# Kernel optimization log

Measured on AMD Instinct MI355X. Metric: run time of the kernel, lower is better.

The kernel has to match this reference:

```python
import jax, jax.numpy as jnp
import numpy as np

D_MODEL = 1024
N_HEADS = 16
HEAD_DIM = D_MODEL // N_HEADS
D_FF = 4096
EPS = 1e-5
THETA = 10000.0
B, S = 2, 2048


def _rope_cache(seq_len, head_dim, theta=THETA):
    inv_freq = 1.0 / theta ** (jnp.arange(0, head_dim, 2, dtype=jnp.float32) / head_dim)
    t = jnp.arange(seq_len, dtype=jnp.float32)
    freqs = jnp.einsum('i,j->ij', t, inv_freq)          # [S, head_dim//2]
    emb = jnp.concatenate([freqs, freqs], axis=-1)       # [S, head_dim]
    return jnp.cos(emb), jnp.sin(emb)


def _rotate_half(x):
    x1, x2 = jnp.split(x, 2, axis=-1)
    return jnp.concatenate([-x2, x1], axis=-1)


def _ada_rmsnorm(x, time_emb, weight, w1, b1, w2, b2):
    # time_mlp: Linear -> SiLU -> Linear producing [B, 2*D]
    h = jax.nn.silu(time_emb @ w1 + b1)
    scale, shift = jnp.split(h @ w2 + b2, 2, axis=-1)    # each [B, D]
    norm = x * jax.lax.rsqrt(jnp.mean(x * x, axis=-1, keepdims=True) + EPS)
    return norm * weight * (1.0 + scale[:, None, :]) + shift[:, None, :]


def setup_inputs() -> dict:
    key = jax.random.key(0)
    ks = jax.random.split(key, 24)
    rn = lambda k, shp: (jax.random.normal(k, shp, dtype=jnp.float32) * 0.02)
    return {
        'x': jax.random.normal(ks[0], (B, S, D_MODEL), dtype=jnp.float32),
        'time_emb': jax.random.normal(ks[1], (B, D_MODEL), dtype=jnp.float32),
        # norm1
        'w_norm1': jnp.ones((D_MODEL,), jnp.float32),
        't1_w1': rn(ks[2], (D_MODEL, D_MODEL)), 't1_b1': jnp.zeros((D_MODEL,), jnp.float32),
        't1_w2': rn(ks[3], (D_MODEL, 2 * D_MODEL)), 't1_b2': jnp.zeros((2 * D_MODEL,), jnp.float32),
        # norm2
        'w_norm2': jnp.ones((D_MODEL,), jnp.float32),
        't2_w1': rn(ks[4], (D_MODEL, D_MODEL)), 't2_b1': jnp.zeros((D_MODEL,), jnp.float32),
        't2_w2': rn(ks[5], (D_MODEL, 2 * D_MODEL)), 't2_b2': jnp.zeros((2 * D_MODEL,), jnp.float32),
        # attention projections (stored [in, out])
        'wq': rn(ks[6], (D_MODEL, D_MODEL)), 'bq': jnp.zeros((D_MODEL,), jnp.float32),
        'wk': rn(ks[7], (D_MODEL, D_MODEL)), 'bk': jnp.zeros((D_MODEL,), jnp.float32),
        'wv': rn(ks[8], (D_MODEL, D_MODEL)), 'bv': jnp.zeros((D_MODEL,), jnp.float32),
        'wo': rn(ks[9], (D_MODEL, D_MODEL)), 'bo': jnp.zeros((D_MODEL,), jnp.float32),
        # GLU FFN (no bias)
        'w_gate': rn(ks[10], (D_MODEL, D_FF)),
        'w_up': rn(ks[11], (D_MODEL, D_FF)),
        'w_down': rn(ks[12], (D_FF, D_MODEL)),
    }


def reference(x, time_emb,
              w_norm1, t1_w1, t1_b1, t1_w2, t1_b2,
              w_norm2, t2_w1, t2_b1, t2_w2, t2_b2,
              wq, bq, wk, bk, wv, bv, wo, bo,
              w_gate, w_up, w_down):
    b, s, _ = x.shape
    cos, sin = _rope_cache(s, HEAD_DIM)                  # [S, head_dim]

    # --- attention sub-block ---
    nx = _ada_rmsnorm(x, time_emb, w_norm1, t1_w1, t1_b1, t1_w2, t1_b2)
    q = (nx @ wq + bq).reshape(b, s, N_HEADS, HEAD_DIM)
    k = (nx @ wk + bk).reshape(b, s, N_HEADS, HEAD_DIM)
    v = (nx @ wv + bv).reshape(b, s, N_HEADS, HEAD_DIM)
    c = cos[:, None, :]  # [S,1,head_dim] broadcasts over heads
    si = sin[:, None, :]
    q = q * c + _rotate_half(q) * si
    k = k * c + _rotate_half(k) * si
    scores = jnp.einsum('bshd,bthd->bhst', q, k) / jnp.sqrt(jnp.float32(HEAD_DIM))
    probs = jax.nn.softmax(scores, axis=-1)
    attn = jnp.einsum('bhst,bthd->bshd', probs, v).reshape(b, s, D_MODEL)
    x = x + attn @ wo + bo

    # --- GLU FFN sub-block ---
    nx = _ada_rmsnorm(x, time_emb, w_norm2, t2_w1, t2_b1, t2_w2, t2_b2)
    gate = jax.nn.gelu(nx @ w_gate, approximate=False)
    ff = (gate * (nx @ w_up)) @ w_down
    return x + ff
```

## Files before the change

### kernel.cpp

```cpp
#include <hip/hip_runtime.h>
#include <hip/hip_bf16.h>

typedef __bf16 bf16_t;
typedef __bf16 bf16x8 __attribute__((ext_vector_type(8)));
typedef float f32x4 __attribute__((ext_vector_type(4)));

typedef __attribute__((address_space(3))) void lds_void_t;
typedef const __attribute__((address_space(1))) void gbl_void_t;

static constexpr int S_LEN = 2048;
static constexpr int NBATCH = 2;
static constexpr int DM = 1024;
static constexpr int NH = 16;
static constexpr int HD = 64;
static constexpr int DFF = 4096;
static constexpr int MROWS = NBATCH * S_LEN;
static constexpr int QKVN = 3072;

__global__ __launch_bounds__(256) void rope_table_k(float* __restrict__ cs) {
  int idx = blockIdx.x * 256 + threadIdx.x;
  int i = idx & 31, s = idx >> 5;
  float inv = powf(10000.0f, -(float)i / 32.0f);
  float ang = (float)s * inv;
  float c = cosf(ang), sn = sinf(ang);
  cs[s * 64 + i] = c;  cs[s * 64 + i + 32] = c;
  cs[S_LEN * 64 + s * 64 + i] = sn;  cs[S_LEN * 64 + s * 64 + i + 32] = sn;
}

__global__ __launch_bounds__(256) void gemv_k(const float* __restrict__ vin,
    const float* __restrict__ W, const float* __restrict__ bias,
    float* __restrict__ out, int N, int dosilu) {
  int b = blockIdx.y;
  int tj = threadIdx.x & 31, ti = threadIdx.x >> 5;
  int j = blockIdx.x * 32 + tj;
  const float* v = vin + b * DM;
  float acc = 0.f;
  int i0 = ti * 128;
#pragma unroll 8
  for (int i = i0; i < i0 + 128; ++i) acc += v[i] * W[(size_t)i * N + j];
  __shared__ float red[8][32];
  red[ti][tj] = acc;
  __syncthreads();
  if (threadIdx.x < 32) {
    float a = 0.f;
#pragma unroll
    for (int t = 0; t < 8; ++t) a += red[t][threadIdx.x];
    a += bias[j - tj + threadIdx.x];
    if (dosilu) a = a / (1.0f + expf(-a));
    out[(size_t)b * N + blockIdx.x * 32 + threadIdx.x] = a;
  }
}

__global__ __launch_bounds__(256) void bcat_k(const float* __restrict__ bq,
    const float* __restrict__ bk, const float* __restrict__ bv, float* __restrict__ o) {
  int i = blockIdx.x * 256 + threadIdx.x;
  o[i] = i < 1024 ? bq[i] : (i < 2048 ? bk[i - 1024] : bv[i - 2048]);
}

template<typename T>
__global__ __launch_bounds__(256) void ada_rms_k(const T* __restrict__ x,
    const float* __restrict__ wnorm, const float* __restrict__ ss,
    bf16_t* __restrict__ out) {
  int row = blockIdx.x;
  int b = row >> 11;
  const T* xr = x + (size_t)row * DM;
  float xl[4]; float s = 0.f;
#pragma unroll
  for (int i = 0; i < 4; ++i) { xl[i] = (float)xr[threadIdx.x + i * 256]; s += xl[i] * xl[i]; }
#pragma unroll
  for (int d = 1; d < 64; d <<= 1) s += __shfl_xor(s, d);
  __shared__ float red[4];
  int w = threadIdx.x >> 6;
  if ((threadIdx.x & 63) == 0) red[w] = s;
  __syncthreads();
  s = red[0] + red[1] + red[2] + red[3];
  float r = rsqrtf(s * (1.0f / DM) + 1e-5f);
  bf16_t* orow = out + (size_t)row * DM;
#pragma unroll
  for (int i = 0; i < 4; ++i) {
    int j = threadIdx.x + i * 256;
    float sc = ss[b * 2048 + j], sh = ss[b * 2048 + 1024 + j];
    orow[j] = (bf16_t)(xl[i] * r * wnorm[j] * (1.0f + sc) + sh);
  }
}

__global__ __launch_bounds__(256) void conv_t_k(const float* __restrict__ in,
    bf16_t* __restrict__ out, int K, int N, int ilv) {
  __shared__ float t[32][33];
  int n0 = blockIdx.x * 32, k0 = blockIdx.y * 32;
  int tx = threadIdx.x & 31, ty = threadIdx.x >> 5;
#pragma unroll
  for (int i = 0; i < 32; i += 8)
    t[ty + i][tx] = in[(size_t)(k0 + ty + i) * N + n0 + tx];
  __syncthreads();
#pragma unroll
  for (int i = 0; i < 32; i += 8) {
    int n = n0 + ty + i;
    int row = (ilv == 0) ? n : ((n >> 4) * 32 + (n & 15) + (ilv == 2 ? 16 : 0));
    out[(size_t)row * K + k0 + tx] = (bf16_t)t[tx][ty + i];
  }
}

template<int EPI, int BK>
__global__ __launch_bounds__(256) void gemm_bt(
    const bf16_t* __restrict__ A, const bf16_t* __restrict__ BT,
    int M, int N, int K,
    const float* __restrict__ bias, const float* __restrict__ residf,
    const bf16_t* __restrict__ residb, bf16_t* outb, float* outf,
    const float* __restrict__ cstab, bf16_t* __restrict__ vt) {
  constexpr int DB = (BK == 64) ? 1 : 2;
  const int col0 = blockIdx.x * 128, row0 = blockIdx.y * 128;
  const int tid = threadIdx.x, l = tid & 63, w = tid >> 6;
  const int wr = (w >> 1) * 64, wc = (w & 1) * 64;
  const int lo = l & 15, hi = l >> 4;
  __shared__ __align__(16) bf16_t lA[DB][128][BK];
  __shared__ __align__(16) bf16_t lB[DB][128][BK];
  f32x4 zero = {0.f, 0.f, 0.f, 0.f};
  f32x4 acc[4][4];
#pragma unroll
  for (int m = 0; m < 4; ++m)
#pragma unroll
    for (int n = 0; n < 4; ++n) acc[m][n] = zero;

  auto stage = [&](int buf, int k0) {
    if constexpr (BK == 64) {
      const int lrow = l >> 3;
      const int swzb = ((l & 7) ^ lrow) * 16;
#pragma unroll
      for (int i = 0; i < 4; ++i) {
        int rbase = w * 32 + i * 8;
        const char* gA = (const char*)&A[(size_t)(row0 + rbase + lrow) * K + k0] + swzb;
        const char* gB = (const char*)&BT[(size_t)(col0 + rbase + lrow) * K + k0] + swzb;
        __builtin_amdgcn_global_load_lds((gbl_void_t*)gA, (lds_void_t*)&lA[buf][rbase][0], 16, 0, 0);
        __builtin_amdgcn_global_load_lds((gbl_void_t*)gB, (lds_void_t*)&lB[buf][rbase][0], 16, 0, 0);
      }
    } else {
      const int lrow = l >> 4;
#pragma unroll
      for (int i = 0; i < 8; ++i) {
        int rbase = w * 32 + i * 4;
        int key = (i * 4 + lrow) & 15;
        int swzb = ((l & 15) ^ key) * 16;
        const char* gA = (const char*)&A[(size_t)(row0 + rbase + lrow) * K + k0] + swzb;
        const char* gB = (const char*)&BT[(size_t)(col0 + rbase + lrow) * K + k0] + swzb;
        __builtin_amdgcn_global_load_lds((gbl_void_t*)gA, (lds_void_t*)&lA[buf][rbase][0], 16, 0, 0);
        __builtin_amdgcn_global_load_lds((gbl_void_t*)gB, (lds_void_t*)&lB[buf][rbase][0], 16, 0, 0);
      }
    }
  };

  const int cmask = (BK == 64) ? (lo & 7) : lo;
  const int NT = K / BK;

  auto compute = [&](int buf) {
#pragma unroll
    for (int kk = 0; kk < BK; kk += 32) {
      bf16x8 af[4], bfr[4];
#pragma unroll
      for (int m = 0; m < 4; ++m)
        af[m] = *(const bf16x8*)&lA[buf][wr + m * 16 + lo][(((kk >> 3) + hi) ^ cmask) * 8];
#pragma unroll
      for (int n = 0; n < 4; ++n)
        bfr[n] = *(const bf16x8*)&lB[buf][wc + n * 16 + lo][(((kk >> 3) + hi) ^ cmask) * 8];
#pragma unroll
      for (int m = 0; m < 4; ++m)
#pragma unroll
        for (int n = 0; n < 4; ++n)
          acc[m][n] = __builtin_amdgcn_mfma_f32_16x16x32_bf16(af[m], bfr[n], acc[m][n], 0, 0, 0);
    }
  };

  if constexpr (DB == 1) {
    for (int t = 0; t < NT; ++t) {
      __syncthreads();
      stage(0, t * BK);
      __syncthreads();
      compute(0);
    }
  } else {
    stage(0, 0);
    __syncthreads();
    int cur = 0;
    for (int t = 0; t < NT; ++t) {
      if (t + 1 < NT) stage(cur ^ 1, (t + 1) * BK);
      compute(cur);
      __syncthreads();
      cur ^= 1;
    }
  }

  if (EPI == 5) {
    if (col0 >= 2048) {
#pragma unroll
      for (int m = 0; m < 4; ++m) {
#pragma unroll
        for (int n = 0; n < 4; ++n) {
          int cl = col0 + wc + n * 16 + lo;
          int r0 = row0 + wr + m * 16 + hi * 4;
          int dfull = cl - 2048;
          int bh = (r0 >> 11) * 16 + (dfull >> 6);
          int d = dfull & 63;
          float bb = bias[cl];
          __align__(8) bf16_t tmp[4];
#pragma unroll
          for (int j = 0; j < 4; ++j) tmp[j] = (bf16_t)(acc[m][n][j] + bb);
          *(uint2*)&vt[((size_t)bh * 64 + d) * S_LEN + (r0 & 2047)] = *(uint2*)tmp;
        }
      }
    } else {
#pragma unroll
      for (int m = 0; m < 4; ++m) {
#pragma unroll
        for (int n = 0; n < 2; ++n) {
          int cl = col0 + wc + n * 16 + lo;
          int i = cl & 63;
          float b1 = bias[cl], b2 = bias[cl + 32];
          float scale = (cl < 1024) ? 0.125f : 1.0f;
#pragma unroll
          for (int j = 0; j < 4; ++j) {
            int r = row0 + wr + m * 16 + hi * 4 + j;
            int s = r & 2047;
            float c = cstab[s * 64 + i], sn = cstab[S_LEN * 64 + s * 64 + i];
            float x1 = acc[m][n][j] + b1, x2 = acc[m][n + 2][j] + b2;
            size_t idx = (size_t)r * N + cl;
            outb[idx]      = (bf16_t)((x1 * c - x2 * sn) * scale);
            outb[idx + 32] = (bf16_t)((x2 * c + x1 * sn) * scale);
          }
        }
      }
    }
    return;
  }

  if (EPI == 6) {
#pragma unroll
    for (int m = 0; m < 4; ++m) {
#pragma unroll
      for (int p = 0; p < 2; ++p) {
        int clg = col0 + wc + 2 * p * 16;
        int jcol = ((clg >> 5) << 4) + lo;
#pragma unroll
        for (int j = 0; j < 4; ++j) {
          int r = row0 + wr + m * 16 + hi * 4 + j;
          float g = acc[m][2 * p][j];
          float u = acc[m][2 * p + 1][j];
          g = 0.5f * g * (1.0f + erff(g * 0.70710678118f));
          outb[(size_t)r * DFF + jcol] = (bf16_t)(g * u);
        }
      }
    }
    return;
  }

#pragma unroll
  for (int m = 0; m < 4; ++m) {
#pragma unroll
    for (int n = 0; n < 4; ++n) {
#pragma unroll
      for (int j = 0; j < 4; ++j) {
        int r = row0 + wr + m * 16 + hi * 4 + j;
        int cl = col0 + wc + n * 16 + lo;
        size_t idx = (size_t)r * N + cl;
        float vv = acc[m][n][j];
        if (EPI == 1)      { vv += bias[cl] + residf[idx]; outb[idx] = (bf16_t)vv; }
        else               { vv += (float)residb[idx]; outf[idx] = vv; }
      }
    }
  }
}

__global__ __launch_bounds__(512, 4) void attn_k(const bf16_t* __restrict__ qk,
    const bf16_t* __restrict__ vt, bf16_t* __restrict__ o) {
  int g = blockIdx.x;
  int orig = (g & 7) * 64 + (g >> 3);
  int qblk = orig & 15;
  int bh = orig >> 4;
  int b = bh >> 4, h = bh & 15;
  const int q0 = qblk * 128;
  const int tid = threadIdx.x, l = tid & 63, w = tid >> 6;
  const int lo = l & 15, hi = l >> 4;

  __shared__ __align__(16) bf16_t lk[128][72];
  __shared__ __align__(16) bf16_t lvt[64][136];
  __shared__ __align__(16) bf16_t lp[8][16][136];

  bf16x8 qf[2];
#pragma unroll
  for (int ks = 0; ks < 2; ++ks)
    qf[ks] = *(const bf16x8*)&qk[((size_t)(b * S_LEN) + q0 + w * 16 + lo) * QKVN
                                 + h * HD + ks * 32 + hi * 8];

  f32x4 zero = {0.f, 0.f, 0.f, 0.f};
  f32x4 oa[4];
#pragma unroll
  for (int n = 0; n < 4; ++n) oa[n] = zero;
  float mrow[4], lrow[4];
#pragma unroll
  for (int j = 0; j < 4; ++j) { mrow[j] = -1e30f; lrow[j] = 0.f; }

  const size_t kbase = (size_t)(b * S_LEN) * QKVN + 1024 + h * HD;
  const size_t vbase = (size_t)bh * 64 * S_LEN;

  for (int t0 = 0; t0 < S_LEN; t0 += 128) {
    __syncthreads();
#pragma unroll
    for (int it = 0; it < 2; ++it) {
      int idx = it * 512 + tid;
      int r = idx >> 3, dc = (idx & 7) * 8;
      *(uint4*)&lk[r][dc] = *(const uint4*)&qk[kbase + (size_t)(t0 + r) * QKVN + dc];
      int d = idx >> 4, sc = (idx & 15) * 8;
      *(uint4*)&lvt[d][sc] = *(const uint4*)&vt[vbase + (size_t)d * S_LEN + t0 + sc];
    }
    __syncthreads();

    f32x4 s[8];
#pragma unroll
    for (int n = 0; n < 8; ++n) s[n] = zero;
    __builtin_amdgcn_s_setprio(1);
#pragma unroll
    for (int ks = 0; ks < 2; ++ks) {
#pragma unroll
      for (int n = 0; n < 8; ++n) {
        bf16x8 bk = *(const bf16x8*)&lk[n * 16 + lo][ks * 32 + hi * 8];
        s[n] = __builtin_amdgcn_mfma_f32_16x16x32_bf16(qf[ks], bk, s[n], 0, 0, 0);
      }
    }
    __builtin_amdgcn_s_setprio(0);

#pragma unroll
    for (int j = 0; j < 4; ++j) {
      float mx = fmaxf(fmaxf(fmaxf(s[0][j], s[1][j]), fmaxf(s[2][j], s[3][j])),
                       fmaxf(fmaxf(s[4][j], s[5][j]), fmaxf(s[6][j], s[7][j])));
      mx = fmaxf(mx, __shfl_xor(mx, 1));
      mx = fmaxf(mx, __shfl_xor(mx, 2));
      mx = fmaxf(mx, __shfl_xor(mx, 4));
      mx = fmaxf(mx, __shfl_xor(mx, 8));
      if (__any(mx > mrow[j] + 8.0f)) {
        float mn = fmaxf(mrow[j], mx);
        float corr = __expf(mrow[j] - mn);
        mrow[j] = mn;
        lrow[j] *= corr;
#pragma unroll
        for (int n = 0; n < 4; ++n) oa[n][j] *= corr;
      }
      float psum = 0.f;
#pragma unroll
      for (int n = 0; n < 8; ++n) {
        float p = __expf(s[n][j] - mrow[j]);
        psum += p;
        lp[w][hi * 4 + j][n * 16 + lo] = (bf16_t)p;
      }
      lrow[j] += psum;
    }

    __builtin_amdgcn_s_setprio(1);
#pragma unroll
    for (int kk = 0; kk < 128; kk += 32) {
      bf16x8 ap = *(const bf16x8*)&lp[w][lo][kk + hi * 8];
#pragma unroll
      for (int n = 0; n < 4; ++n) {
        bf16x8 bv = *(const bf16x8*)&lvt[n * 16 + lo][kk + hi * 8];
        oa[n] = __builtin_amdgcn_mfma_f32_16x16x32_bf16(ap, bv, oa[n], 0, 0, 0);
      }
    }
    __builtin_amdgcn_s_setprio(0);
  }

#pragma unroll
  for (int j = 0; j < 4; ++j) {
    float ls = lrow[j];
    ls += __shfl_xor(ls, 1); ls += __shfl_xor(ls, 2);
    ls += __shfl_xor(ls, 4); ls += __shfl_xor(ls, 8);
    float inv = 1.0f / ls;
    int row = q0 + w * 16 + hi * 4 + j;
#pragma unroll
    for (int n = 0; n < 4; ++n)
      o[((size_t)(b * S_LEN) + row) * DM + h * HD + n * 16 + lo] = (bf16_t)(oa[n][j] * inv);
  }
}

extern "C" void kernel_launch(void* const* d_in, const int* in_sizes, int n_in,
                              void* d_out, int out_size, void* d_ws, size_t ws_size,
                              hipStream_t stream) {
  const float* x    = (const float*)d_in[0];
  const float* te   = (const float*)d_in[1];
  const float* wn1  = (const float*)d_in[2];
  const float* t1w1 = (const float*)d_in[3];
  const float* t1b1 = (const float*)d_in[4];
  const float* t1w2 = (const float*)d_in[5];
  const float* t1b2 = (const float*)d_in[6];
  const float* wn2  = (const float*)d_in[7];
  const float* t2w1 = (const float*)d_in[8];
  const float* t2b1 = (const float*)d_in[9];
  const float* t2w2 = (const float*)d_in[10];
  const float* t2b2 = (const float*)d_in[11];
  const float* wq   = (const float*)d_in[12];
  const float* bq   = (const float*)d_in[13];
  const float* wk   = (const float*)d_in[14];
  const float* bk   = (const float*)d_in[15];
  const float* wv   = (const float*)d_in[16];
  const float* bv   = (const float*)d_in[17];
  const float* wo   = (const float*)d_in[18];
  const float* bo   = (const float*)d_in[19];
  const float* wg   = (const float*)d_in[20];
  const float* wu   = (const float*)d_in[21];
  const float* wd   = (const float*)d_in[22];
  float* out = (float*)d_out;

  char* ws = (char*)d_ws;
  const size_t MB = 1ull << 20;
  bf16_t* woT   = (bf16_t*)(ws + 0 * MB);
  bf16_t* wguT  = (bf16_t*)(ws + 2 * MB);
  bf16_t* wdT   = (bf16_t*)(ws + 18 * MB);
  bf16_t* nx    = (bf16_t*)(ws + 26 * MB);
  bf16_t* wqkvT = (bf16_t*)(ws + 34 * MB);
  bf16_t* qkvb  = (bf16_t*)(ws + 40 * MB);
  bf16_t* vt    = (bf16_t*)(ws + 64 * MB);
  bf16_t* gb    = (bf16_t*)(ws + 40 * MB);
  bf16_t* attnb = (bf16_t*)(ws + 72 * MB);
  bf16_t* x2b   = (bf16_t*)(ws + 80 * MB);
  float*  cs    = (float*)(ws + 88 * MB);
  float*  ss1   = (float*)(ws + 89 * MB);
  float*  ss2   = (float*)(ws + 89 * MB + 16384);
  float*  htmp  = (float*)(ws + 89 * MB + 32768);
  float*  bcat  = (float*)(ws + 89 * MB + 40960);

  rope_table_k<<<256, 256, 0, stream>>>(cs);
  bcat_k<<<12, 256, 0, stream>>>(bq, bk, bv, bcat);
  gemv_k<<<dim3(32, 2), 256, 0, stream>>>(te, t1w1, t1b1, htmp, 1024, 1);
  gemv_k<<<dim3(64, 2), 256, 0, stream>>>(htmp, t1w2, t1b2, ss1, 2048, 0);
  gemv_k<<<dim3(32, 2), 256, 0, stream>>>(te, t2w1, t2b1, htmp, 1024, 1);
  gemv_k<<<dim3(64, 2), 256, 0, stream>>>(htmp, t2w2, t2b2, ss2, 2048, 0);

  conv_t_k<<<dim3(32, 32),  256, 0, stream>>>(wq, wqkvT,               1024, 1024, 0);
  conv_t_k<<<dim3(32, 32),  256, 0, stream>>>(wk, wqkvT + 1024 * 1024, 1024, 1024, 0);
  conv_t_k<<<dim3(32, 32),  256, 0, stream>>>(wv, wqkvT + 2048 * 1024, 1024, 1024, 0);
  conv_t_k<<<dim3(32, 32),  256, 0, stream>>>(wo, woT, 1024, 1024, 0);
  conv_t_k<<<dim3(128, 32), 256, 0, stream>>>(wg, wguT, 1024, 4096, 1);
  conv_t_k<<<dim3(128, 32), 256, 0, stream>>>(wu, wguT, 1024, 4096, 2);
  conv_t_k<<<dim3(32, 128), 256, 0, stream>>>(wd, wdT, 4096, 1024, 0);

  ada_rms_k<float><<<MROWS, 256, 0, stream>>>(x, wn1, ss1, nx);

  gemm_bt<5, 64><<<dim3(24, 32), 256, 0, stream>>>(nx, wqkvT, MROWS, QKVN, DM,
                                                   bcat, nullptr, nullptr, qkvb, nullptr, cs, vt);

  attn_k<<<512, 512, 0, stream>>>(qkvb, vt, attnb);

  gemm_bt<1, 128><<<dim3(8, 32), 256, 0, stream>>>(attnb, woT, MROWS, DM, DM,
                                                   bo, x, nullptr, x2b, nullptr, nullptr, nullptr);

  ada_rms_k<bf16_t><<<MROWS, 256, 0, stream>>>(x2b, wn2, ss2, nx);

  gemm_bt<6, 64><<<dim3(64, 32), 256, 0, stream>>>(nx, wguT, MROWS, 2 * DFF, DM,
                                                   nullptr, nullptr, nullptr, gb, nullptr, nullptr, nullptr);
  gemm_bt<4, 128><<<dim3(8, 32), 256, 0, stream>>>(gb, wdT, MROWS, DM, DFF,
                                                   nullptr, nullptr, x2b, nullptr, out, nullptr, nullptr);
}
```

Before: 357.9 us.

## Merge weight transpose and bias concat into one prep kernel, precompute GEMM load pointers

Replaces seven conv_t_k launches and the bcat_k launch with a single prep_k launch that picks its weight matrix and tile from the block index. This removes per-launch overhead and the tail gaps between small kernels. The GEMM main loops now keep precomputed global source pointers and advance them each K step instead of recomputing addresses. The GEMM also gets a launch_bounds occupancy hint (4 blocks for BK=64, 1 for BK=128), which could change register allocation.

```diff
diff --git a/kernel.cpp b/kernel.cpp
--- a/kernel.cpp
+++ b/kernel.cpp
@@ -51,12 +51,6 @@
   }
 }
 
-__global__ __launch_bounds__(256) void bcat_k(const float* __restrict__ bq,
-    const float* __restrict__ bk, const float* __restrict__ bv, float* __restrict__ o) {
-  int i = blockIdx.x * 256 + threadIdx.x;
-  o[i] = i < 1024 ? bq[i] : (i < 2048 ? bk[i - 1024] : bv[i - 2048]);
-}
-
 template<typename T>
 __global__ __launch_bounds__(256) void ada_rms_k(const T* __restrict__ x,
     const float* __restrict__ wnorm, const float* __restrict__ ss,
@@ -84,25 +78,51 @@
   }
 }
 
-__global__ __launch_bounds__(256) void conv_t_k(const float* __restrict__ in,
-    bf16_t* __restrict__ out, int K, int N, int ilv) {
-  __shared__ float t[32][33];
-  int n0 = blockIdx.x * 32, k0 = blockIdx.y * 32;
+__global__ __launch_bounds__(256) void prep_k(
+    const float* __restrict__ wq, const float* __restrict__ wk,
+    const float* __restrict__ wv, const float* __restrict__ wo,
+    const float* __restrict__ wg, const float* __restrict__ wu,
+    const float* __restrict__ wd,
+    bf16_t* __restrict__ wqkvT, bf16_t* __restrict__ woT,
+    bf16_t* __restrict__ wguT, bf16_t* __restrict__ wdT,
+    const float* __restrict__ bq, const float* __restrict__ bk,
+    const float* __restrict__ bv, float* __restrict__ bcat) {
+  int id = blockIdx.x;
+  if (id >= 16384) {
+    int i = (id - 16384) * 256 + threadIdx.x;
+    if (i < 3072)
+      bcat[i] = i < 1024 ? bq[i] : (i < 2048 ? bk[i - 1024] : bv[i - 2048]);
+    return;
+  }
+  const float* in; bf16_t* outp; int K, N, ilv, t;
+  if (id < 4096) {
+    int j = id >> 10; t = id & 1023; K = 1024; N = 1024; ilv = 0;
+    in   = j == 0 ? wq : j == 1 ? wk : j == 2 ? wv : wo;
+    outp = j == 3 ? woT : wqkvT + (size_t)j * 1024 * 1024;
+  } else if (id < 12288) {
+    int j = (id - 4096) >> 12; t = (id - 4096) & 4095; K = 1024; N = 4096;
+    ilv = 1 + j; in = j ? wu : wg; outp = wguT;
+  } else {
+    t = id - 12288; K = 4096; N = 1024; ilv = 0; in = wd; outp = wdT;
+  }
+  int nbx = N >> 5;
+  int n0 = (t % nbx) * 32, k0 = (t / nbx) * 32;
+  __shared__ float tl[32][33];
   int tx = threadIdx.x & 31, ty = threadIdx.x >> 5;
 #pragma unroll
   for (int i = 0; i < 32; i += 8)
-    t[ty + i][tx] = in[(size_t)(k0 + ty + i) * N + n0 + tx];
+    tl[ty + i][tx] = in[(size_t)(k0 + ty + i) * N + n0 + tx];
   __syncthreads();
 #pragma unroll
   for (int i = 0; i < 32; i += 8) {
     int n = n0 + ty + i;
     int row = (ilv == 0) ? n : ((n >> 4) * 32 + (n & 15) + (ilv == 2 ? 16 : 0));
-    out[(size_t)row * K + k0 + tx] = (bf16_t)t[tx][ty + i];
+    outp[(size_t)row * K + k0 + tx] = (bf16_t)tl[tx][ty + i];
   }
 }
 
 template<int EPI, int BK>
-__global__ __launch_bounds__(256) void gemm_bt(
+__global__ __launch_bounds__(256, (BK == 64) ? 4 : 1) void gemm_bt(
     const bf16_t* __restrict__ A, const bf16_t* __restrict__ BT,
     int M, int N, int K,
     const float* __restrict__ bias, const float* __restrict__ residf,
@@ -122,67 +142,74 @@
 #pragma unroll
     for (int n = 0; n < 4; ++n) acc[m][n] = zero;
 
-  auto stage = [&](int buf, int k0) {
-    if constexpr (BK == 64) {
-      const int lrow = l >> 3;
-      const int swzb = ((l & 7) ^ lrow) * 16;
+  const int cmask = (BK == 64) ? (lo & 7) : lo;
+  const int NT = K / BK;
+
+  auto compute = [&](int buf) {
+#pragma unroll
+    for (int kk = 0; kk < BK; kk += 32) {
+      bf16x8 af[4], bfr[4];
+#pragma unroll
+      for (int m = 0; m < 4; ++m)
+        af[m] = *(const bf16x8*)&lA[buf][wr + m * 16 + lo][(((kk >> 3) + hi) ^ cmask) * 8];
+#pragma unroll
+      for (int n = 0; n < 4; ++n)
+        bfr[n] = *(const bf16x8*)&lB[buf][wc + n * 16 + lo][(((kk >> 3) + hi) ^ cmask) * 8];
+#pragma unroll
+      for (int m = 0; m < 4; ++m)
+#pragma unroll
+        for (int n = 0; n < 4; ++n)
+          acc[m][n] = __builtin_amdgcn_mfma_f32_16x16x32_bf16(af[m], bfr[n], acc[m][n], 0, 0, 0);
+    }
+  };
+
+  if constexpr (DB == 1) {
+    const int lrow = l >> 3;
+    const int swzb = ((l & 7) ^ lrow) * 16;
+    const char* pA[4]; const char* pB[4];
+#pragma unroll
+    for (int i = 0; i < 4; ++i) {
+      int rbase = w * 32 + i * 8;
+      pA[i] = (const char*)&A[(size_t)(row0 + rbase + lrow) * K] + swzb;
+      pB[i] = (const char*)&BT[(size_t)(col0 + rbase + lrow) * K] + swzb;
+    }
+    for (int t = 0; t < NT; ++t) {
+      __syncthreads();
 #pragma unroll
       for (int i = 0; i < 4; ++i) {
         int rbase = w * 32 + i * 8;
-        const char* gA = (const char*)&A[(size_t)(row0 + rbase + lrow) * K + k0] + swzb;
-        const char* gB = (const char*)&BT[(size_t)(col0 + rbase + lrow) * K + k0] + swzb;
-        __builtin_amdgcn_global_load_lds((gbl_void_t*)gA, (lds_void_t*)&lA[buf][rbase][0], 16, 0, 0);
-        __builtin_amdgcn_global_load_lds((gbl_void_t*)gB, (lds_void_t*)&lB[buf][rbase][0], 16, 0, 0);
-      }
-    } else {
-      const int lrow = l >> 4;
+        __builtin_amdgcn_global_load_lds((gbl_void_t*)pA[i], (lds_void_t*)&lA[0][rbase][0], 16, 0, 0);
+        __builtin_amdgcn_global_load_lds((gbl_void_t*)pB[i], (lds_void_t*)&lB[0][rbase][0], 16, 0, 0);
+        pA[i] += 128; pB[i] += 128;
+      }
+      __syncthreads();
+      compute(0);
+    }
+  } else {
+    const int lrow = l >> 4;
+    const char* pA[8]; const char* pB[8];
+#pragma unroll
+    for (int i = 0; i < 8; ++i) {
+      int rbase = w * 32 + i * 4;
+      int key = (i * 4 + lrow) & 15;
+      int swzb = ((l & 15) ^ key) * 16;
+      pA[i] = (const char*)&A[(size_t)(row0 + rbase + lrow) * K] + swzb;
+      pB[i] = (const char*)&BT[(size_t)(col0 + rbase + lrow) * K] + swzb;
+    }
+    auto stage_p = [&](int buf) {
 #pragma unroll
       for (int i = 0; i < 8; ++i) {
         int rbase = w * 32 + i * 4;
-        int key = (i * 4 + lrow) & 15;
-        int swzb = ((l & 15) ^ key) * 16;
-        const char* gA = (const char*)&A[(size_t)(row0 + rbase + lrow) * K + k0] + swzb;
-        const char* gB = (const char*)&BT[(size_t)(col0 + rbase + lrow) * K + k0] + swzb;
-        __builtin_amdgcn_global_load_lds((gbl_void_t*)gA, (lds_void_t*)&lA[buf][rbase][0], 16, 0, 0);
-        __builtin_amdgcn_global_load_lds((gbl_void_t*)gB, (lds_void_t*)&lB[buf][rbase][0], 16, 0, 0);
-      }
-    }
-  };
-
-  const int cmask = (BK == 64) ? (lo & 7) : lo;
-  const int NT = K / BK;
-
-  auto compute = [&](int buf) {
-#pragma unroll
-    for (int kk = 0; kk < BK; kk += 32) {
-      bf16x8 af[4], bfr[4];
-#pragma unroll
-      for (int m = 0; m < 4; ++m)
-        af[m] = *(const bf16x8*)&lA[buf][wr + m * 16 + lo][(((kk >> 3) + hi) ^ cmask) * 8];
-#pragma unroll
-      for (int n = 0; n < 4; ++n)
-        bfr[n] = *(const bf16x8*)&lB[buf][wc + n * 16 + lo][(((kk >> 3) + hi) ^ cmask) * 8];
-#pragma unroll
-      for (int m = 0; m < 4; ++m)
-#pragma unroll
-        for (int n = 0; n < 4; ++n)
-          acc[m][n] = __builtin_amdgcn_mfma_f32_16x16x32_bf16(af[m], bfr[n], acc[m][n], 0, 0, 0);
-    }
-  };
-
-  if constexpr (DB == 1) {
-    for (int t = 0; t < NT; ++t) {
-      __syncthreads();
-      stage(0, t * BK);
-      __syncthreads();
-      compute(0);
-    }
-  } else {
-    stage(0, 0);
+        __builtin_amdgcn_global_load_lds((gbl_void_t*)pA[i], (lds_void_t*)&lA[buf][rbase][0], 16, 0, 0);
+        __builtin_amdgcn_global_load_lds((gbl_void_t*)pB[i], (lds_void_t*)&lB[buf][rbase][0], 16, 0, 0);
+        pA[i] += 256; pB[i] += 256;
+      }
+    };
+    stage_p(0);
     __syncthreads();
     int cur = 0;
     for (int t = 0; t < NT; ++t) {
-      if (t + 1 < NT) stage(cur ^ 1, (t + 1) * BK);
+      if (t + 1 < NT) stage_p(cur ^ 1);
       compute(cur);
       __syncthreads();
       cur ^= 1;
@@ -426,19 +453,13 @@
   float*  bcat  = (float*)(ws + 89 * MB + 40960);
 
   rope_table_k<<<256, 256, 0, stream>>>(cs);
-  bcat_k<<<12, 256, 0, stream>>>(bq, bk, bv, bcat);
   gemv_k<<<dim3(32, 2), 256, 0, stream>>>(te, t1w1, t1b1, htmp, 1024, 1);
   gemv_k<<<dim3(64, 2), 256, 0, stream>>>(htmp, t1w2, t1b2, ss1, 2048, 0);
   gemv_k<<<dim3(32, 2), 256, 0, stream>>>(te, t2w1, t2b1, htmp, 1024, 1);
   gemv_k<<<dim3(64, 2), 256, 0, stream>>>(htmp, t2w2, t2b2, ss2, 2048, 0);
 
-  conv_t_k<<<dim3(32, 32),  256, 0, stream>>>(wq, wqkvT,               1024, 1024, 0);
-  conv_t_k<<<dim3(32, 32),  256, 0, stream>>>(wk, wqkvT + 1024 * 1024, 1024, 1024, 0);
-  conv_t_k<<<dim3(32, 32),  256, 0, stream>>>(wv, wqkvT + 2048 * 1024, 1024, 1024, 0);
-  conv_t_k<<<dim3(32, 32),  256, 0, stream>>>(wo, woT, 1024, 1024, 0);
-  conv_t_k<<<dim3(128, 32), 256, 0, stream>>>(wg, wguT, 1024, 4096, 1);
-  conv_t_k<<<dim3(128, 32), 256, 0, stream>>>(wu, wguT, 1024, 4096, 2);
-  conv_t_k<<<dim3(32, 128), 256, 0, stream>>>(wd, wdT, 4096, 1024, 0);
+  prep_k<<<16396, 256, 0, stream>>>(wq, wk, wv, wo, wg, wu, wd,
+                                    wqkvT, woT, wguT, wdT, bq, bk, bv, bcat);
 
   ada_rms_k<float><<<MROWS, 256, 0, stream>>>(x, wn1, ss1, nx);
 
```

Measured after the change: 324.6 us. -9.3%, faster.
